# Kernel tuning notes

Hardware: AMD Instinct MI355X
Metric: run time of the kernel (lower is better)

The kernel has to match this reference:

```python
import jax, jax.numpy as jnp
import numpy as np

D_MODEL = 2048
FFN_MULT = 4
N_ROUTED = 8
TOP_K = 2
H_ROUTED = FFN_MULT * D_MODEL // N_ROUTED   # 1024
H_SHARED = FFN_MULT * D_MODEL               # 8192


def setup_inputs() -> dict:
    key = jax.random.key(0)
    ks = jax.random.split(key, 8)
    s = 0.02
    x = jax.random.normal(ks[0], (4, 2048, D_MODEL), dtype=jnp.float32)
    w_gate = jax.random.normal(ks[1], (N_ROUTED, D_MODEL), dtype=jnp.float32) * s
    Wg = jax.random.normal(ks[2], (N_ROUTED, D_MODEL, H_ROUTED), dtype=jnp.float32) * s
    Wu = jax.random.normal(ks[3], (N_ROUTED, D_MODEL, H_ROUTED), dtype=jnp.float32) * s
    Wd = jax.random.normal(ks[4], (N_ROUTED, H_ROUTED, D_MODEL), dtype=jnp.float32) * s
    Sg = jax.random.normal(ks[5], (D_MODEL, H_SHARED), dtype=jnp.float32) * s
    Su = jax.random.normal(ks[6], (D_MODEL, H_SHARED), dtype=jnp.float32) * s
    Sd = jax.random.normal(ks[7], (H_SHARED, D_MODEL), dtype=jnp.float32) * s
    return {"x": x, "w_gate": w_gate, "Wg": Wg, "Wu": Wu, "Wd": Wd,
            "Sg": Sg, "Su": Su, "Sd": Sd}


def reference(x, w_gate, Wg, Wu, Wd, Sg, Su, Sd):
    B, T, D = x.shape
    N = B * T
    xf = x.reshape(N, D)

    # shared expert (n_shared = 1)
    shared = (jax.nn.silu(xf @ Sg) * (xf @ Su)) @ Sd          # [N, D]

    # gate (eval mode: clean logits, no noise)
    clean = xf @ w_gate.T                                      # [N, E]
    top_logits, top_idx = jax.lax.top_k(clean, TOP_K)          # [N, K]
    gates = jax.nn.softmax(top_logits, axis=-1)                # [N, K]
    # load-balance loss
    importance = jax.nn.softmax(clean, axis=-1).sum(0)         # [E]
    ce = importance / N * N_ROUTED
    lb_loss = jnp.mean(ce * ce)

    # combine weights: combine[n,e] = sum_k gates[n,k] * (top_idx[n,k]==e)
    onehot = jax.nn.one_hot(top_idx, N_ROUTED, dtype=xf.dtype)  # [N, K, E]
    combine = jnp.einsum('nke,nk->ne', onehot, gates)           # [N, E]

    # routed experts (dense grouped form, zero-weight tokens contribute 0)
    hg = jnp.einsum('nd,edh->neh', xf, Wg)
    hu = jnp.einsum('nd,edh->neh', xf, Wu)
    h = jax.nn.silu(hg) * hu                                    # [N, E, H]
    routed = jnp.einsum('neh,ehd,ne->nd', h, Wd, combine)       # [N, D]

    out = (shared + routed).reshape(B, T, D)
    return out, lb_loss
```

## Files before the change

kernel.cpp:

```cpp
#include <hip/hip_runtime.h>
#include <hip/hip_bf16.h>
#include <hip/hip_fp16.h>
#include <stdint.h>

#define NTOK   8192
#define DM     2048
#define NEXP   8
#define HR     1024
#define HS     8192
#define ROWS_MAX 18432

typedef _Float16 f16;
typedef f16  f16x8 __attribute__((ext_vector_type(8)));
typedef float f32x4 __attribute__((ext_vector_type(4)));

#define GLP(p) ((const __attribute__((address_space(1))) void*)(p))
#define LDP(p) ((__attribute__((address_space(3))) void*)(p))

static __device__ __forceinline__ float silu_f(float v) {
  return v / (1.0f + __expf(-v));
}

static __device__ __forceinline__ int xcd_swz(int bid, int nwg) {
  const int q = nwg >> 3, r = nwg & 7;
  const int x = bid & 7, i = bid >> 3;
  return (x < r ? x * (q + 1) : r * (q + 1) + (x - r) * q) + i;
}


__global__ __launch_bounds__(256)
void conv_all_kernel(const float* __restrict__ Sg, const float* __restrict__ Su,
                     const float* __restrict__ Sd, const float* __restrict__ Wg,
                     const float* __restrict__ Wu, const float* __restrict__ Wd,
                     f16* __restrict__ SguI, f16* __restrict__ SdT,
                     f16* __restrict__ WguI, f16* __restrict__ WdT) {
  __shared__ float t[32][33];
  const int bid = blockIdx.x;
  const int s = bid >> 14, rr = bid & 16383;
  const float* in;
  f16* outb;
  int C, xbits, rmap;
  int b = 0, tile = rr;
  if (s >= 3) { b = rr >> 11; tile = rr & 2047; }
  switch (s) {
    case 0:  in = Sg; outb = SguI; C = HS; xbits = 8; rmap = 1; break;
    case 1:  in = Su; outb = SguI; C = HS; xbits = 8; rmap = 2; break;
    case 2:  in = Sd; outb = SdT;  C = DM; xbits = 6; rmap = 0; break;
    case 3:  in = Wg + (size_t)b * DM * HR; outb = WguI + (size_t)b * 2048 * DM;
             C = HR; xbits = 5; rmap = 1; break;
    case 4:  in = Wu + (size_t)b * DM * HR; outb = WguI + (size_t)b * 2048 * DM;
             C = HR; xbits = 5; rmap = 2; break;
    default: in = Wd + (size_t)b * HR * DM; outb = WdT + (size_t)b * DM * HR;
             C = DM; xbits = 6; rmap = 0; break;
  }
  const int c0 = (tile & ((1 << xbits) - 1)) << 5;
  const int r0 = (tile >> xbits) << 5;
  const int R_out = C;
  const int tx = threadIdx.x, ty0 = threadIdx.y;
#pragma unroll
  for (int yy = 0; yy < 4; ++yy) {
    const int ty = ty0 + yy * 8;
    t[ty][tx] = in[(size_t)(r0 + ty) * C + (c0 + tx)];
  }
  __syncthreads();
  const int R = (s == 2) ? HS : ((s == 5) ? HR : DM);
  (void)R_out;
#pragma unroll
  for (int yy = 0; yy < 4; ++yy) {
    const int ty = ty0 + yy * 8;
    const int tr = c0 + ty;
    const int pr = rmap ? (((tr >> 4) << 5) + ((rmap - 1) << 4) + (tr & 15)) : tr;
    outb[(size_t)pr * R + (r0 + tx)] = (f16)t[tx][ty];
  }
}


__global__ __launch_bounds__(256)
void gate_kernel(const float* __restrict__ x, const float* __restrict__ wgate,
                 f16* __restrict__ x16, float* __restrict__ gateW,
                 int* __restrict__ gateI, float* __restrict__ importance,
                 int* __restrict__ cnt) {
  __shared__ float impl[NEXP];
  __shared__ int cntl[NEXP];
  const int tid = threadIdx.x, lane = tid & 63, wid = tid >> 6;
  if (tid < NEXP) { impl[tid] = 0.f; cntl[tid] = 0; }
  __syncthreads();
  for (int s = 0; s < 8; ++s) {
    const int t = blockIdx.x * 32 + wid * 8 + s;
    const float* xr = x + (size_t)t * DM;
    f16* x16r = x16 + (size_t)t * DM;
    float pv[NEXP] = {0.f, 0.f, 0.f, 0.f, 0.f, 0.f, 0.f, 0.f};
    for (int j = 0; j < DM / 64; ++j) {
      const int c = lane + j * 64;
      const float xv = xr[c];
      x16r[c] = (f16)xv;
#pragma unroll
      for (int e = 0; e < NEXP; ++e) pv[e] += xv * wgate[e * DM + c];
    }
#pragma unroll
    for (int e = 0; e < NEXP; ++e) {
#pragma unroll
      for (int st = 32; st >= 1; st >>= 1) pv[e] += __shfl_xor(pv[e], st);
    }
    if (lane == 0) {
      float v1 = pv[0]; int i1 = 0;
#pragma unroll
      for (int e = 1; e < NEXP; ++e) if (pv[e] > v1) { v1 = pv[e]; i1 = e; }
      float v2 = -1e30f; int i2 = 0;
#pragma unroll
      for (int e = 0; e < NEXP; ++e) if (e != i1 && pv[e] > v2) { v2 = pv[e]; i2 = e; }
      const float g1 = 1.f / (1.f + expf(v2 - v1));
      gateW[t * 2 + 0] = g1;  gateW[t * 2 + 1] = 1.f - g1;
      gateI[t * 2 + 0] = i1;  gateI[t * 2 + 1] = i2;
      float mx = pv[0];
#pragma unroll
      for (int e = 1; e < NEXP; ++e) mx = fmaxf(mx, pv[e]);
      float sum = 0.f, ex[NEXP];
#pragma unroll
      for (int e = 0; e < NEXP; ++e) { ex[e] = expf(pv[e] - mx); sum += ex[e]; }
      const float inv = 1.f / sum;
#pragma unroll
      for (int e = 0; e < NEXP; ++e) atomicAdd(&impl[e], ex[e] * inv);
      atomicAdd(&cntl[i1], 1);
      atomicAdd(&cntl[i2], 1);
    }
  }
  __syncthreads();
  if (tid < NEXP) {
    atomicAdd(&importance[tid], impl[tid]);
    atomicAdd(&cnt[tid], cntl[tid]);
  }
}

__global__ void scan_kernel(const int* __restrict__ cnt, int* __restrict__ seg,
                            int* __restrict__ cursor, const float* __restrict__ imp,
                            float* __restrict__ lb_out) {
  if (threadIdx.x == 0 && blockIdx.x == 0) {
    int o = 0;
#pragma unroll
    for (int e = 0; e < NEXP; ++e) {
      seg[e] = o;
      o += (cnt[e] + 255) & ~255;
      cursor[e] = 0;
    }
    seg[NEXP] = o;
    float s = 0.f;
#pragma unroll
    for (int e = 0; e < NEXP; ++e) {
      const float ce = imp[e] * ((float)NEXP / (float)NTOK);
      s += ce * ce;
    }
    *lb_out = s / (float)NEXP;
  }
}

__global__ __launch_bounds__(256)
void scatter_kernel(const float* __restrict__ gateW, const int* __restrict__ gateI,
                    const int* __restrict__ seg, int* __restrict__ cursor,
                    int* __restrict__ rowtok, float* __restrict__ rowgate) {
  const int t = blockIdx.x * 256 + threadIdx.x;
  const int lane = threadIdx.x & 63;
#pragma unroll
  for (int k = 0; k < 2; ++k) {
    const int e = gateI[t * 2 + k];
    const float g = gateW[t * 2 + k];
    for (int ee = 0; ee < NEXP; ++ee) {
      const unsigned long long m = __ballot(e == ee);
      if (e == ee) {
        const int leader = __ffsll((unsigned long long)m) - 1;
        const int rank = (int)__popcll(m & ((1ull << lane) - 1ull));
        int base = 0;
        if (lane == leader) base = atomicAdd(&cursor[ee], (int)__popcll(m));
        base = __shfl(base, leader);
        const int pos = seg[ee] + base + rank;
        rowtok[pos] = t;
        rowgate[pos] = g;
      }
    }
  }
}


struct G8Ptrs { const f16* a[4]; const f16* b[4]; };

static __device__ __forceinline__ void swz_rc(int tid, int i, int& r, int& c) {
  const int L = i * 8192 + tid * 16;
  const int U = L ^ (((L >> 7) & 7) << 4);
  r = U >> 7;
  c = (U & 127) >> 1;
}

static __device__ __forceinline__ void stage8(const G8Ptrs& P, int koff,
                                              f16* AsB, f16* BsB, int wid) {
#pragma unroll
  for (int i = 0; i < 4; ++i) {
    __builtin_amdgcn_global_load_lds(GLP(P.a[i] + koff), LDP(AsB + i * 4096 + wid * 512), 16, 0, 0);
    __builtin_amdgcn_global_load_lds(GLP(P.b[i] + koff), LDP(BsB + i * 4096 + wid * 512), 16, 0, 0);
  }
}

static __device__ __forceinline__ void g8_mainloop(const G8Ptrs& P, int nt,
                                                   f16* As, f16* Bs,
                                                   f32x4 (&acc)[8][4]) {
  const int tid = threadIdx.x;
  const int lane = tid & 63, wid = tid >> 6;
  const int wr = wid >> 2, wc = wid & 3;
  const int fr = lane & 15, fk = (lane >> 4) * 8;

  stage8(P, 0, As, Bs, wid);
  asm volatile("s_waitcnt vmcnt(0)" ::: "memory");
  __syncthreads();

  for (int t = 0; t < nt; ++t) {
    const int cur = t & 1;
    if (t + 1 < nt)
      stage8(P, (t + 1) * 64, As + (cur ^ 1) * 16384, Bs + (cur ^ 1) * 16384, wid);
    const f16* Ab = As + cur * 16384;
    const f16* Bb = Bs + cur * 16384;
    f16x8 bf[4][2];
#pragma unroll
    for (int n = 0; n < 4; ++n) {
      const int r = wc * 64 + n * 16 + fr;
      const int sw = (r & 7) << 3;
#pragma unroll
      for (int ks = 0; ks < 2; ++ks)
        bf[n][ks] = *(const f16x8*)&Bb[(r * 64 + ks * 32 + fk) ^ sw];
    }
#pragma unroll
    for (int mh = 0; mh < 2; ++mh) {
#pragma unroll
      for (int ks = 0; ks < 2; ++ks) {
        f16x8 af[4];
#pragma unroll
        for (int m = 0; m < 4; ++m) {
          const int r = wr * 128 + (mh * 4 + m) * 16 + fr;
          af[m] = *(const f16x8*)&Ab[(r * 64 + ks * 32 + fk) ^ ((r & 7) << 3)];
        }
#pragma unroll
        for (int m = 0; m < 4; ++m)
#pragma unroll
          for (int n = 0; n < 4; ++n)
            acc[mh * 4 + m][n] =
                __builtin_amdgcn_mfma_f32_16x16x32_f16(af[m], bf[n][ks], acc[mh * 4 + m][n], 0, 0, 0);
      }
    }
    asm volatile("s_waitcnt vmcnt(0)" ::: "memory");
    __syncthreads();
  }
}

__global__ __launch_bounds__(512, 2)
void g8_gu(const f16* __restrict__ A, const f16* __restrict__ B,
           f16* __restrict__ H, int gx, int Nh, int K) {
  __shared__ f16 As[2 * 16384], Bs[2 * 16384];
  const int lin = xcd_swz(blockIdx.x, gridDim.x);
  const int row0 = (lin % gx) * 256, n0 = (lin / gx) * 256;
  const int tid = threadIdx.x;
  G8Ptrs P;
#pragma unroll
  for (int i = 0; i < 4; ++i) {
    int r, c; swz_rc(tid, i, r, c);
    P.a[i] = A + (size_t)(row0 + r) * K + c;
    P.b[i] = B + (size_t)(n0 + r) * K + c;
  }
  f32x4 acc[8][4] = {};
  g8_mainloop(P, K / 64, As, Bs, acc);
  const int lane = tid & 63, wid = tid >> 6;
  const int wr = wid >> 2, wc = wid & 3;
  const int fr = lane & 15, r0 = (lane >> 4) * 4;
  const int hc0 = (n0 + wc * 64) >> 1;
#pragma unroll
  for (int m = 0; m < 8; ++m)
#pragma unroll
    for (int k = 0; k < 2; ++k)
#pragma unroll
      for (int rr = 0; rr < 4; ++rr) {
        const int row = row0 + wr * 128 + m * 16 + r0 + rr;
        const int hcol = hc0 + k * 16 + fr;
        const float g = acc[m][2 * k][rr];
        const float u = acc[m][2 * k + 1][rr];
        H[(size_t)row * Nh + hcol] = (f16)(silu_f(g) * u);
      }
}

__global__ __launch_bounds__(512, 2)
void g8_down(const f16* __restrict__ A, const f16* __restrict__ B,
             float* __restrict__ out, int gx, int N, int K) {
  __shared__ f16 As[2 * 16384], Bs[2 * 16384];
  const int lin = xcd_swz(blockIdx.x, gridDim.x);
  const int row0 = (lin % gx) * 256, n0 = (lin / gx) * 256;
  const int tid = threadIdx.x;
  G8Ptrs P;
#pragma unroll
  for (int i = 0; i < 4; ++i) {
    int r, c; swz_rc(tid, i, r, c);
    P.a[i] = A + (size_t)(row0 + r) * K + c;
    P.b[i] = B + (size_t)(n0 + r) * K + c;
  }
  f32x4 acc[8][4] = {};
  g8_mainloop(P, K / 64, As, Bs, acc);
  const int lane = tid & 63, wid = tid >> 6;
  const int wr = wid >> 2, wc = wid & 3;
  const int fr = lane & 15, r0 = (lane >> 4) * 4;
#pragma unroll
  for (int m = 0; m < 8; ++m)
#pragma unroll
    for (int n = 0; n < 4; ++n)
#pragma unroll
      for (int rr = 0; rr < 4; ++rr) {
        const int row = row0 + wr * 128 + m * 16 + r0 + rr;
        const int col = n0 + wc * 64 + n * 16 + fr;
        out[(size_t)row * N + col] = acc[m][n][rr];
      }
}

__global__ __launch_bounds__(512, 2)
void g8_rgu(const f16* __restrict__ x16, const int* __restrict__ rowtok,
            const f16* __restrict__ Wgu, f16* __restrict__ hr,
            const int* __restrict__ seg) {
  __shared__ f16 As[2 * 16384], Bs[2 * 16384];
  const int e = blockIdx.z;
  const int row0 = seg[e] + blockIdx.y * 256;
  if (row0 >= seg[e + 1]) return;
  const int n0 = blockIdx.x * 256;
  const f16* Bbase = Wgu + (size_t)e * 2048 * DM;
  const int tid = threadIdx.x;
  G8Ptrs P;
#pragma unroll
  for (int i = 0; i < 4; ++i) {
    int r, c; swz_rc(tid, i, r, c);
    int tok = rowtok[row0 + r];
    if (tok < 0) tok = 0;
    P.a[i] = x16 + (size_t)tok * DM + c;
    P.b[i] = Bbase + (size_t)(n0 + r) * DM + c;
  }
  f32x4 acc[8][4] = {};
  g8_mainloop(P, DM / 64, As, Bs, acc);
  const int lane = tid & 63, wid = tid >> 6;
  const int wr = wid >> 2, wc = wid & 3;
  const int fr = lane & 15, r0 = (lane >> 4) * 4;
  const int hc0 = (n0 + wc * 64) >> 1;
#pragma unroll
  for (int m = 0; m < 8; ++m)
#pragma unroll
    for (int k = 0; k < 2; ++k)
#pragma unroll
      for (int rr = 0; rr < 4; ++rr) {
        const int row = row0 + wr * 128 + m * 16 + r0 + rr;
        const int hcol = hc0 + k * 16 + fr;
        const float g = acc[m][2 * k][rr];
        const float u = acc[m][2 * k + 1][rr];
        hr[(size_t)row * HR + hcol] = (f16)(silu_f(g) * u);
      }
}

__global__ __launch_bounds__(512, 2)
void g8_rdown(const f16* __restrict__ A, const f16* __restrict__ B,
              float* __restrict__ out, const int* __restrict__ seg,
              const int* __restrict__ rowtok, const float* __restrict__ rowgate) {
  __shared__ f16 As[2 * 16384], Bs[2 * 16384];
  const int e = blockIdx.z;
  const int row0 = seg[e] + blockIdx.y * 256;
  if (row0 >= seg[e + 1]) return;
  const int n0 = blockIdx.x * 256;
  const f16* Bbase = B + (size_t)e * DM * HR;
  const int tid = threadIdx.x;
  G8Ptrs P;
#pragma unroll
  for (int i = 0; i < 4; ++i) {
    int r, c; swz_rc(tid, i, r, c);
    P.a[i] = A + (size_t)(row0 + r) * HR + c;
    P.b[i] = Bbase + (size_t)(n0 + r) * HR + c;
  }
  f32x4 acc[8][4] = {};
  g8_mainloop(P, HR / 64, As, Bs, acc);
  const int lane = tid & 63, wid = tid >> 6;
  const int wr = wid >> 2, wc = wid & 3;
  const int fr = lane & 15, r0 = (lane >> 4) * 4;
#pragma unroll
  for (int m = 0; m < 8; ++m)
#pragma unroll
    for (int rr = 0; rr < 4; ++rr) {
      const int pos = row0 + wr * 128 + m * 16 + r0 + rr;
      const int tok = rowtok[pos];
      if (tok >= 0) {
        const float gw = rowgate[pos];
#pragma unroll
        for (int n = 0; n < 4; ++n) {
          const int col = n0 + wc * 64 + n * 16 + fr;
          atomicAdd(&out[(size_t)tok * DM + col], acc[m][n][rr] * gw);
        }
      }
    }
}


extern "C" void kernel_launch(void* const* d_in, const int* in_sizes, int n_in,
                              void* d_out, int out_size, void* d_ws, size_t ws_size,
                              hipStream_t stream) {
  const float* x  = (const float*)d_in[0];
  const float* wg = (const float*)d_in[1];
  const float* Wg = (const float*)d_in[2];
  const float* Wu = (const float*)d_in[3];
  const float* Wd = (const float*)d_in[4];
  const float* Sg = (const float*)d_in[5];
  const float* Su = (const float*)d_in[6];
  const float* Sd = (const float*)d_in[7];
  float* out = (float*)d_out;

  char* p = (char*)d_ws;
  auto take = [&](size_t b) { char* q = p; p += (b + 255) & ~(size_t)255; return q; };
  float* importance = (float*)take(32);
  int*   cnt        = (int*)take(32);
  int*   cursor     = (int*)take(32);
  int*   seg        = (int*)take(64);
  int*   rowtok     = (int*)take((size_t)ROWS_MAX * 4);
  float* rowgate    = (float*)take((size_t)ROWS_MAX * 4);
  float* gateW      = (float*)take((size_t)NTOK * 2 * 4);
  int*   gateI      = (int*)take((size_t)NTOK * 2 * 4);
  f16* x16   = (f16*)take((size_t)NTOK * DM * 2);
  f16* SguI  = (f16*)take((size_t)2 * HS * DM * 2);
  f16* SdT   = (f16*)take((size_t)DM * HS * 2);
  f16* WguI  = (f16*)take((size_t)NEXP * 2048 * DM * 2);
  f16* WdT   = (f16*)take((size_t)NEXP * DM * HR * 2);
  f16* hbuf  = (f16*)take((size_t)NTOK * HS * 2);
  f16* hr    = (f16*)take((size_t)ROWS_MAX * HR * 2);
  if ((size_t)(p - (char*)d_ws) > ws_size) return;

  hipMemsetAsync(importance, 0, 768, stream);
  hipMemsetAsync(rowtok, 0xFF, (size_t)ROWS_MAX * 4, stream);

  gate_kernel<<<NTOK / 32, 256, 0, stream>>>(x, wg, x16, gateW, gateI, importance, cnt);
  scan_kernel<<<1, 64, 0, stream>>>(cnt, seg, cursor, importance, out + (size_t)NTOK * DM);
  scatter_kernel<<<NTOK / 256, 256, 0, stream>>>(gateW, gateI, seg, cursor, rowtok, rowgate);

  conv_all_kernel<<<6 * 16384, dim3(32, 8), 0, stream>>>(Sg, Su, Sd, Wg, Wu, Wd,
                                                         SguI, SdT, WguI, WdT);

  g8_rgu<<<dim3(8, 33, NEXP), 512, 0, stream>>>(x16, rowtok, WguI, hr, seg);

  g8_gu<<<32 * 64, 512, 0, stream>>>(x16, SguI, hbuf, 32, HS, DM);
  g8_down<<<32 * 8, 512, 0, stream>>>(hbuf, SdT, out, 32, DM, HS);

  g8_rdown<<<dim3(8, 33, NEXP), 512, 0, stream>>>(hr, WdT, out, seg, rowtok, rowgate);
}
```

Measured before the change: 1.414 ms.

## Rewrite shared gate-up GEMM mainloop with finer-grained staged LDS pipeline

Replaces the generic mainloop in the shared-expert gate/up GEMM with a specialized loop that splits each 64-wide K tile into two 32-wide halves. Global-to-LDS loads of upcoming halves are interleaved between MFMA groups, and MFMA bursts are raised with s_setprio. Dimensions are hard-coded as compile-time constants. The LDS layout drops the XOR swizzle in favor of plain 32-element rows, which may add bank conflicts on fragment reads in exchange for simpler addressing and finer overlap of loads with compute.

```diff
diff --git a/kernel.cpp b/kernel.cpp
--- a/kernel.cpp
+++ b/kernel.cpp
@@ -55,7 +55,6 @@
   }
   const int c0 = (tile & ((1 << xbits) - 1)) << 5;
   const int r0 = (tile >> xbits) << 5;
-  const int R_out = C;
   const int tx = threadIdx.x, ty0 = threadIdx.y;
 #pragma unroll
   for (int yy = 0; yy < 4; ++yy) {
@@ -64,7 +63,6 @@
   }
   __syncthreads();
   const int R = (s == 2) ? HS : ((s == 5) ? HR : DM);
-  (void)R_out;
 #pragma unroll
   for (int yy = 0; yy < 4; ++yy) {
     const int ty = ty0 + yy * 8;
@@ -249,22 +247,96 @@
   }
 }
 
+
+static __device__ __forceinline__ void g8_mainloop8(
+    const f16* __restrict__ aR0, const f16* __restrict__ aR1,
+    const f16* __restrict__ bR0, const f16* __restrict__ bR1,
+    int nt, f16* As, f16* Bs, f32x4 (&acc)[8][4]) {
+  const int tid = threadIdx.x;
+  const int lane = tid & 63, wid = tid >> 6;
+  const int wr = wid >> 2, wc = wid & 3;
+  const int fr = lane & 15, fk2 = (lane >> 4) * 8;
+
+#define UOFF8(j) ((((j) >> 1) & 1) * 16384 + ((j) & 1) * 8192 + tid * 8)
+#define STGA8(j) do { if ((j) < 2 * nt) { \
+    __builtin_amdgcn_global_load_lds(GLP(aR0 + (size_t)(j) * 32), LDP(As + UOFF8(j)), 16, 0, 0); \
+    __builtin_amdgcn_global_load_lds(GLP(aR1 + (size_t)(j) * 32), LDP(As + UOFF8(j) + 4096), 16, 0, 0); } } while (0)
+#define STGB8(j) do { if ((j) < 2 * nt) { \
+    __builtin_amdgcn_global_load_lds(GLP(bR0 + (size_t)(j) * 32), LDP(Bs + UOFF8(j)), 16, 0, 0); \
+    __builtin_amdgcn_global_load_lds(GLP(bR1 + (size_t)(j) * 32), LDP(Bs + UOFF8(j) + 4096), 16, 0, 0); } } while (0)
+#define LOADBF8(Bb) _Pragma("unroll") \
+    for (int n = 0; n < 4; ++n) { \
+      const int r = wc * 64 + n * 16 + fr; \
+      bf[n] = *(const f16x8*)&(Bb)[r * 32 + fk2]; }
+#define LOADAF8(Ab, MH) _Pragma("unroll") \
+    for (int m = 0; m < 4; ++m) { \
+      const int r = wr * 128 + ((MH) * 4 + m) * 16 + fr; \
+      af[m] = *(const f16x8*)&(Ab)[r * 32 + fk2]; }
+#define MFMA16(MH) \
+    __builtin_amdgcn_s_barrier(); \
+    asm volatile("s_waitcnt lgkmcnt(0)" ::: "memory"); \
+    __builtin_amdgcn_sched_barrier(0); \
+    __builtin_amdgcn_s_setprio(1); \
+    _Pragma("unroll") \
+    for (int m = 0; m < 4; ++m) \
+      _Pragma("unroll") \
+      for (int n = 0; n < 4; ++n) \
+        acc[(MH) * 4 + m][n] = __builtin_amdgcn_mfma_f32_16x16x32_f16(af[m], bf[n], acc[(MH) * 4 + m][n], 0, 0, 0); \
+    __builtin_amdgcn_s_setprio(0);
+
+  STGA8(0); STGB8(0); STGA8(1); STGB8(1); STGA8(2); STGB8(2);
+  asm volatile("s_waitcnt vmcnt(4)" ::: "memory");
+  __builtin_amdgcn_s_barrier();
+
+  f16x8 af[4], bf[4];
+  for (int t = 0; t < nt; ++t) {
+    const f16* Ab = As + (t & 1) * 16384;
+    const f16* Bb = Bs + (t & 1) * 16384;
+    STGA8(2 * t + 3);
+    LOADBF8(Bb);
+    LOADAF8(Ab, 0);
+    MFMA16(0);
+    __builtin_amdgcn_s_barrier();
+    STGB8(2 * t + 3);
+    LOADAF8(Ab, 1);
+    MFMA16(1);
+    __builtin_amdgcn_s_barrier();
+    STGA8(2 * t + 4);
+    LOADBF8(Bb + 8192);
+    LOADAF8(Ab + 8192, 0);
+    MFMA16(0);
+    __builtin_amdgcn_s_barrier();
+    STGB8(2 * t + 4);
+    LOADAF8(Ab + 8192, 1);
+    MFMA16(1);
+    if (t + 1 < nt) {
+      if (t + 2 < nt) { asm volatile("s_waitcnt vmcnt(4)" ::: "memory"); }
+      else            { asm volatile("s_waitcnt vmcnt(0)" ::: "memory"); }
+      __builtin_amdgcn_s_barrier();
+    }
+  }
+#undef UOFF8
+#undef STGA8
+#undef STGB8
+#undef LOADBF8
+#undef LOADAF8
+#undef MFMA16
+}
+
 __global__ __launch_bounds__(512, 2)
 void g8_gu(const f16* __restrict__ A, const f16* __restrict__ B,
-           f16* __restrict__ H, int gx, int Nh, int K) {
-  __shared__ f16 As[2 * 16384], Bs[2 * 16384];
-  const int lin = xcd_swz(blockIdx.x, gridDim.x);
-  const int row0 = (lin % gx) * 256, n0 = (lin / gx) * 256;
+           f16* __restrict__ H) {
+  __shared__ f16 As[32768], Bs[32768];
+  const int lin = xcd_swz(blockIdx.x, 2048);
+  const int row0 = (lin % 32) * 256, n0 = (lin / 32) * 256;
   const int tid = threadIdx.x;
-  G8Ptrs P;
-#pragma unroll
-  for (int i = 0; i < 4; ++i) {
-    int r, c; swz_rc(tid, i, r, c);
-    P.a[i] = A + (size_t)(row0 + r) * K + c;
-    P.b[i] = B + (size_t)(n0 + r) * K + c;
-  }
+  const int rs = tid >> 2, kws = (tid & 3) * 8;
+  const f16* aR0 = A + (size_t)(row0 + rs) * DM + kws;
+  const f16* aR1 = A + (size_t)(row0 + rs + 128) * DM + kws;
+  const f16* bR0 = B + (size_t)(n0 + rs) * DM + kws;
+  const f16* bR1 = B + (size_t)(n0 + rs + 128) * DM + kws;
   f32x4 acc[8][4] = {};
-  g8_mainloop(P, K / 64, As, Bs, acc);
+  g8_mainloop8(aR0, aR1, bR0, bR1, DM / 64, As, Bs, acc);
   const int lane = tid & 63, wid = tid >> 6;
   const int wr = wid >> 2, wc = wid & 3;
   const int fr = lane & 15, r0 = (lane >> 4) * 4;
@@ -279,7 +351,7 @@
         const int hcol = hc0 + k * 16 + fr;
         const float g = acc[m][2 * k][rr];
         const float u = acc[m][2 * k + 1][rr];
-        H[(size_t)row * Nh + hcol] = (f16)(silu_f(g) * u);
+        H[(size_t)row * HS + hcol] = (f16)(silu_f(g) * u);
       }
 }
 
@@ -439,7 +511,7 @@
 
   g8_rgu<<<dim3(8, 33, NEXP), 512, 0, stream>>>(x16, rowtok, WguI, hr, seg);
 
-  g8_gu<<<32 * 64, 512, 0, stream>>>(x16, SguI, hbuf, 32, HS, DM);
+  g8_gu<<<32 * 64, 512, 0, stream>>>(x16, SguI, hbuf);
   g8_down<<<32 * 8, 512, 0, stream>>>(hbuf, SdT, out, 32, DM, HS);
 
   g8_rdown<<<dim3(8, 33, NEXP), 512, 0, stream>>>(hr, WdT, out, seg, rowtok, rowgate);
```

New measurement: 1.717 ms. 21.4% more time.
